# Kernel tuning notes

Hardware: AMD Instinct MI355X
Metric: run time of the kernel (lower is better)

## Reference

```python
import jax, jax.numpy as jnp
import numpy as np

D_MODEL = 512
EXPAND = 2
D_INNER = D_MODEL * EXPAND      # 1024
STATE = 64                      # N
DT_RANK = D_MODEL // 16         # 32
CONV_K = 4
K_WIN = 8                       # window of the approximate selective scan
LN_EPS = 1e-5


def setup_inputs() -> dict:
    key = jax.random.key(0)
    ks = jax.random.split(key, 8)
    norm = lambda k, shape, scale: (jax.random.normal(k, shape, jnp.float32) * scale)
    return {
        "x": jax.random.normal(ks[0], (1, 1024, D_MODEL), jnp.float32),
        "in_proj_w": norm(ks[1], (2 * D_INNER, D_MODEL), D_MODEL ** -0.5),
        "conv_w": norm(ks[2], (D_INNER, 1, CONV_K), 0.5),            # depthwise [O, I/g=1, K]
        "conv_b": jnp.zeros((D_INNER,), jnp.float32),
        "x_proj_w": norm(ks[3], (DT_RANK + 2 * STATE, D_INNER), D_INNER ** -0.5),
        "dt_proj_w": norm(ks[4], (D_INNER, DT_RANK), DT_RANK ** -0.5),
        "dt_proj_b": jnp.zeros((D_INNER,), jnp.float32),
        "A_log": jnp.broadcast_to(
            jnp.log(jnp.arange(1, STATE + 1, dtype=jnp.float32)), (D_INNER, STATE)
        ) + 0.0,
        "D_param": jnp.ones((D_INNER,), jnp.float32),
        "out_proj_w": norm(ks[5], (D_MODEL, D_INNER), D_INNER ** -0.5),
        "ln_w": jnp.ones((D_MODEL,), jnp.float32),
        "ln_b": jnp.zeros((D_MODEL,), jnp.float32),
    }


def _selective_scan(x, dt, A, Bp, Cp, Dp):
    """Windowed selective scan (faithful to the torch loop, vectorized).

    h_t = sum_{s=max(0,t-K+1)}^{t} exp(sum_{j=s+1}^{t} dt_j * A) * dt_s * B_s * x_s
    y_t = <h_t, C_t> + D * x_t
    x, dt: [B, L, d]; A: [d, N]; Bp, Cp: [B, L, N]; Dp: [d]
    """
    L = x.shape[1]
    K = min(L, K_WIN)
    log_dA = dt[..., None] * A                                # [B,L,d,N], <= 0
    dBx = dt[..., None] * Bp[:, :, None, :] * x[..., None]    # [B,L,d,N]
    cs = jnp.cumsum(log_dA, axis=1)                           # prefix sums of log-decay
    h = dBx
    for k in range(1, K):  # fixed small window, 7 iterations
        decay = jnp.exp(cs[:, k:] - cs[:, :-k])               # prod dA over (t-k, t]
        h = h.at[:, k:].add(decay * dBx[:, :-k])
    y = jnp.einsum('bldn,bln->bld', h, Cp) + Dp * x
    return y


def reference(x, in_proj_w, conv_w, conv_b, x_proj_w, dt_proj_w, dt_proj_b,
              A_log, D_param, out_proj_w, ln_w, ln_b):
    residual = x
    xz = x @ in_proj_w.T                                      # [B,L,2*d_inner]
    x_in, z = jnp.split(xz, 2, axis=-1)

    # causal depthwise conv1d (torch pads 3 both sides then keeps first L)
    xc = jnp.transpose(x_in, (0, 2, 1))                       # [B,d,L]
    xc = jax.lax.conv_general_dilated(
        xc, conv_w, window_strides=(1,), padding=[(CONV_K - 1, 0)],
        dimension_numbers=('NCH', 'OIH', 'NCH'), feature_group_count=D_INNER,
    ) + conv_b[None, :, None]
    xc = jax.nn.silu(jnp.transpose(xc, (0, 2, 1)))            # [B,L,d]

    x_dbl = xc @ x_proj_w.T                                   # [B,L,dt_rank+2N]
    dt, Bp, Cp = jnp.split(x_dbl, [DT_RANK, DT_RANK + STATE], axis=-1)
    dt = jax.nn.softplus(dt @ dt_proj_w.T + dt_proj_b)        # [B,L,d]
    A = -jnp.exp(A_log)                                       # [d,N]

    y = _selective_scan(xc, dt, A, Bp, Cp, D_param)
    y = y * jax.nn.silu(z)
    out = y @ out_proj_w.T + residual

    mu = out.mean(-1, keepdims=True)
    var = ((out - mu) ** 2).mean(-1, keepdims=True)
    return (out - mu) * jax.lax.rsqrt(var + LN_EPS) * ln_w + ln_b
```

## Files before the change

### kernel.cpp

```cpp
#include <hip/hip_runtime.h>
#include <hip/hip_fp16.h>
#include <math.h>

#define LSEQ    1024
#define DMODEL  512
#define DINNER  1024
#define NSTATE  64
#define NFUSED  1152
#define CHUNKT  64
#define PROWS   72
#define NCH     16

#define MB (1024u * 1024u)
#define XZ_OFF      (0)
#define XC_OFF      (8u * MB)
#define XCBF_OFF    (12u * MB)
#define XBF_OFF     (14u * MB)
#define INWBF_OFF   (15u * MB)
#define OUTWBF_OFF  (17u * MB)
#define WF_OFF      (18u * MB)
#define FUSED_OFF   (20u * MB + 256u * 1024)
#define BCHI_OFF    (24u * MB + 768u * 1024)
#define YBF_OFF     (25u * MB)
#define OUTPRE_OFF  (27u * MB)

typedef __attribute__((ext_vector_type(8))) short bf16x8;
typedef __attribute__((ext_vector_type(4))) float f32x4;

__device__ inline unsigned short f2bf(float f) {
  unsigned int u = __float_as_uint(f);
  u += 0x7fff + ((u >> 16) & 1);
  return (unsigned short)(u >> 16);
}
__device__ inline float h2f(unsigned short h) {
  return __half2float(__ushort_as_half(h));
}
__device__ inline float fexp2(float x) { return __builtin_amdgcn_exp2f(x); }

__global__ __launch_bounds__(256) void prep_kernel(
    const float* __restrict__ x, const float* __restrict__ inw,
    const float* __restrict__ outw, const float* __restrict__ xpw,
    const float* __restrict__ dtw, unsigned short* __restrict__ x_bf,
    unsigned short* __restrict__ inw_bf, unsigned short* __restrict__ outw_bf,
    unsigned short* __restrict__ Wf) {
  const int blk = blockIdx.x;
  if (blk < 2048) {
    const int i = blk * 256 + threadIdx.x;
    const float* src;
    unsigned short* dst;
    int j;
    if (i < 131072) {
      src = x; dst = x_bf; j = i;
    } else if (i < 393216) {
      src = inw; dst = inw_bf; j = i - 131072;
    } else {
      src = outw; dst = outw_bf; j = i - 393216;
    }
    const float4 v = *(const float4*)&src[(size_t)j * 4];
    ushort4 o;
    o.x = f2bf(v.x); o.y = f2bf(v.y); o.z = f2bf(v.z); o.w = f2bf(v.w);
    *(ushort4*)&dst[(size_t)j * 4] = o;
  } else {
    const int r = blk - 2048;
    if (r < 128) {
      for (int i = threadIdx.x; i < 1024; i += 256)
        Wf[(size_t)r * 1024 + i] = f2bf(xpw[(size_t)(32 + r) * 1024 + i]);
    } else {
      const int d = r - 128;
      __shared__ float w[32];
      if (threadIdx.x < 32) w[threadIdx.x] = dtw[d * 32 + threadIdx.x];
      __syncthreads();
      for (int i = threadIdx.x; i < 1024; i += 256) {
        float s = 0.f;
#pragma unroll
        for (int q = 0; q < 32; ++q) s = fmaf(w[q], xpw[(size_t)q * 1024 + i], s);
        Wf[(size_t)r * 1024 + i] = f2bf(s);
      }
    }
  }
}

template <int BM, int BN, int WM, int WN, bool RESID, bool WBCH>
__global__ __launch_bounds__(256) void gemm_bf(
    const unsigned short* __restrict__ A, const unsigned short* __restrict__ B,
    float* __restrict__ C, const float* __restrict__ resid,
    unsigned short* __restrict__ bch, int M, int N, int K) {
  constexpr int BK = 64;
  constexpr int WTM = BM / WM;
  constexpr int WTN = BN / WN;
  constexpr int FM = WTM / 16;
  constexpr int FN = WTN / 16;
  constexpr int APASS = (BM * BK * 2) / 4096;
  constexpr int BPASS = (BN * BK * 2) / 4096;

  __shared__ unsigned short As[2][BM * BK];
  __shared__ unsigned short Bs[2][BN * BK];

  const int tid = threadIdx.x;
  const int lane = tid & 63;
  const int wave = tid >> 6;
  const int wr = (wave / WN) * WTM;
  const int wc = (wave % WN) * WTN;
  const int bm = blockIdx.y * BM;
  const int bn = blockIdx.x * BN;

  auto stage = [&](int buf, int kt) {
#pragma unroll
    for (int p = 0; p < APASS; ++p) {
      const int s = tid + p * 256;
      const int row = s >> 3;
      const int sch = (s & 7) ^ (row & 7);
      const unsigned short* src = A + (size_t)(bm + row) * K + kt + sch * 8;
      __builtin_amdgcn_global_load_lds(
          (const __attribute__((address_space(1))) unsigned int*)src,
          (__attribute__((address_space(3))) unsigned int*)(&As[buf][s * 8]),
          16, 0, 0);
    }
#pragma unroll
    for (int p = 0; p < BPASS; ++p) {
      const int s = tid + p * 256;
      const int row = s >> 3;
      const int sch = (s & 7) ^ (row & 7);
      const unsigned short* src = B + (size_t)(bn + row) * K + kt + sch * 8;
      __builtin_amdgcn_global_load_lds(
          (const __attribute__((address_space(1))) unsigned int*)src,
          (__attribute__((address_space(3))) unsigned int*)(&Bs[buf][s * 8]),
          16, 0, 0);
    }
  };

  f32x4 acc[FM][FN];
#pragma unroll
  for (int m = 0; m < FM; ++m)
#pragma unroll
    for (int n = 0; n < FN; ++n) acc[m][n] = (f32x4){0.f, 0.f, 0.f, 0.f};

  const int nt = K / BK;
  stage(0, 0);
  __syncthreads();
  int cur = 0;
  for (int t = 0; t < nt; ++t) {
    if (t + 1 < nt) stage(cur ^ 1, (t + 1) * BK);
#pragma unroll
    for (int kk = 0; kk < BK / 32; ++kk) {
      bf16x8 a[FM], b[FN];
#pragma unroll
      for (int m = 0; m < FM; ++m) {
        const int arow = wr + m * 16 + (lane & 15);
        const int ach = (kk * 4 + (lane >> 4)) ^ (arow & 7);
        a[m] = *(const bf16x8*)(&As[cur][arow * BK + ach * 8]);
      }
#pragma unroll
      for (int n = 0; n < FN; ++n) {
        const int brow = wc + n * 16 + (lane & 15);
        const int bchk = (kk * 4 + (lane >> 4)) ^ (brow & 7);
        b[n] = *(const bf16x8*)(&Bs[cur][brow * BK + bchk * 8]);
      }
#pragma unroll
      for (int m = 0; m < FM; ++m)
#pragma unroll
        for (int n = 0; n < FN; ++n)
          acc[m][n] = __builtin_amdgcn_mfma_f32_16x16x32_bf16(a[m], b[n],
                                                              acc[m][n], 0, 0, 0);
    }
    __syncthreads();
    cur ^= 1;
  }

#pragma unroll
  for (int m = 0; m < FM; ++m)
#pragma unroll
    for (int n = 0; n < FN; ++n) {
      const int col = bn + wc + n * 16 + (lane & 15);
#pragma unroll
      for (int r = 0; r < 4; ++r) {
        const int row = bm + wr + m * 16 + (lane >> 4) * 4 + r;
        float v = acc[m][n][r];
        if (RESID) v += resid[(size_t)row * N + col];
        C[(size_t)row * N + col] = v;
        if (WBCH) {
          if (col < 128) {
            const int j = col & 63, hi = col >> 6;
            bch[(size_t)row * 128 + j * 2 + hi] =
                __half_as_ushort(__float2half(v));
          }
        }
      }
    }
}

__global__ __launch_bounds__(256) void conv_silu_kernel(
    const float* __restrict__ xz, const float* __restrict__ w,
    const float* __restrict__ b, float* __restrict__ xc,
    unsigned short* __restrict__ xc_bf) {
  const int idx = blockIdx.x * 256 + threadIdx.x;
  const int t = idx >> 10;
  const int d = idx & 1023;
  float acc = b[d];
#pragma unroll
  for (int j = 0; j < 4; ++j) {
    const int ts = t - 3 + j;
    if (ts >= 0) acc = fmaf(xz[(size_t)ts * 2048 + d], w[d * 4 + j], acc);
  }
  const float s = acc / (1.f + __expf(-acc));
  xc[idx] = s;
  xc_bf[idx] = f2bf(s);
}

__global__ __launch_bounds__(512) void scan_kernel(
    const float* __restrict__ fused,
    const unsigned int* __restrict__ bchi,
    const float* __restrict__ xc,
    const float* __restrict__ xz,
    const float* __restrict__ A_log,
    const float* __restrict__ dtb,
    const float* __restrict__ Dp,
    unsigned short* __restrict__ y_bf) {
  __shared__ unsigned int bch[PROWS * 64];
  __shared__ float2 dtl[PROWS * NCH];
  __shared__ unsigned int auxl[CHUNKT * NCH];
  __shared__ unsigned short ytile[CHUNKT * NCH];

  const int tid = threadIdx.x;
  const int lane = tid & 63;
  const int wave = tid >> 6;
  const int d0 = blockIdx.x * NCH;
  const int t0 = blockIdx.y * CHUNKT;
  const int T = t0 - 8;

#pragma unroll
  for (int pp = 0; pp < 3; ++pp) {
    const int idx = pp * 512 + tid;
    if (idx < PROWS * 16) {
      const int p = idx >> 4;
      const int c4 = (idx & 15) * 4;
      const int gt = T + p;
      uint4 v = make_uint4(0u, 0u, 0u, 0u);
      if (gt >= 0) v = *(const uint4*)&bchi[(size_t)gt * 64 + c4];
      *(uint4*)&bch[p * 64 + c4] = v;
    }
  }

  if (tid < 4 * PROWS) {
    const int row = tid >> 2;
    const int dloc = (tid & 3) * 4;
    const int gt = T + row;
    if (gt >= 0) {
      const float4 f  = *(const float4*)&fused[(size_t)gt * NFUSED + 128 + d0 + dloc];
      const float4 xv = *(const float4*)&xc[(size_t)gt * DINNER + d0 + dloc];
      const float4 zv = *(const float4*)&xz[(size_t)gt * 2048 + DINNER + d0 + dloc];
      const float4 dp = *(const float4*)&Dp[d0 + dloc];
      const float4 db = *(const float4*)&dtb[d0 + dloc];
      const float fa[4] = {f.x, f.y, f.z, f.w};
      const float xa[4] = {xv.x, xv.y, xv.z, xv.w};
      const float za[4] = {zv.x, zv.y, zv.z, zv.w};
      const float pa[4] = {dp.x, dp.y, dp.z, dp.w};
      const float ba[4] = {db.x, db.y, db.z, db.w};
#pragma unroll
      for (int q = 0; q < 4; ++q) {
        const float dtp = fa[q] + ba[q];
        const float dt = (dtp > 20.f) ? dtp : __logf(1.f + __expf(dtp));
        dtl[row * NCH + dloc + q] = make_float2(dt, dt * xa[q]);
        if (row >= 8) {
          const float dxc = pa[q] * xa[q];
          const float sz = za[q] / (1.f + __expf(-za[q]));
          auxl[(row - 8) * NCH + dloc + q] =
              (unsigned int)__half_as_ushort(__float2half(dxc)) |
              ((unsigned int)__half_as_ushort(__float2half(sz)) << 16);
        }
      }
    } else {
#pragma unroll
      for (int q = 0; q < 4; ++q)
        dtl[row * NCH + dloc + q] = make_float2(0.f, 0.f);
    }
  }
  __syncthreads();

  const int chl = wave * 2;
  const float An2a = -__expf(A_log[(size_t)(d0 + chl) * NSTATE + lane]) * 1.44269504f;
  const float An2b = -__expf(A_log[(size_t)(d0 + chl + 1) * NSTATE + lane]) * 1.44269504f;

  float ERa[8], dBa[8], ERb[8], dBb[8];
#pragma unroll
  for (int p = 0; p < 8; ++p) {
    const float4 pk = *(const float4*)&dtl[p * NCH + chl];
    const float Bp = h2f((unsigned short)(bch[p * 64 + lane] & 0xffffu));
    ERa[p] = fexp2(An2a * pk.x);
    dBa[p] = pk.y * Bp;
    ERb[p] = fexp2(An2b * pk.z);
    dBb[p] = pk.w * Bp;
  }

  for (int sb = 0; sb < CHUNKT; sb += 8) {
#pragma unroll
    for (int qu = 0; qu < 2; ++qu) {
      float cc[8];
#pragma unroll
      for (int h4 = 0; h4 < 4; ++h4) {
        const int u = qu * 4 + h4;
        const int p = sb + 8 + u;
        const float4 pk = *(const float4*)&dtl[p * NCH + chl];
        const unsigned int bc = bch[p * 64 + lane];
        const float Bp = h2f((unsigned short)(bc & 0xffffu));
        const float Cp = h2f((unsigned short)(bc >> 16));
        const float Ea = fexp2(An2a * pk.x);
        const float Eb = fexp2(An2b * pk.z);
        const float dBta = pk.y * Bp;
        const float dBtb = pk.w * Bp;

        float sa = dBa[(u - 7) & 7];
        float sb2 = dBb[(u - 7) & 7];
#pragma unroll
        for (int k = 6; k >= 1; --k) {
          const int sl = (u - k) & 7;
          sa = fmaf(ERa[sl], sa, dBa[sl]);
          sb2 = fmaf(ERb[sl], sb2, dBb[sl]);
        }
        const float ha = fmaf(Ea, sa, dBta);
        const float hb = fmaf(Eb, sb2, dBtb);
        ERa[u] = Ea; dBa[u] = dBta;
        ERb[u] = Eb; dBb[u] = dBtb;
        cc[h4 * 2] = ha * Cp;
        cc[h4 * 2 + 1] = hb * Cp;
      }
      float a[8];
#pragma unroll
      for (int i = 0; i < 8; ++i) a[i] = cc[i] + __shfl_xor(cc[i], 1, 64);
      float b0 = (lane & 1) ? a[1] : a[0];
      float b1 = (lane & 1) ? a[3] : a[2];
      float b2 = (lane & 1) ? a[5] : a[4];
      float b3 = (lane & 1) ? a[7] : a[6];
      b0 += __shfl_xor(b0, 2, 64);
      b1 += __shfl_xor(b1, 2, 64);
      b2 += __shfl_xor(b2, 2, 64);
      b3 += __shfl_xor(b3, 2, 64);
      float c0 = (lane & 2) ? b1 : b0;
      float c1 = (lane & 2) ? b3 : b2;
      c0 += __shfl_xor(c0, 4, 64);
      c1 += __shfl_xor(c1, 4, 64);
      float r = (lane & 4) ? c1 : c0;
      r += __shfl_xor(r, 8, 64);
      r += __shfl_xor(r, 16, 64);
      r += __shfl_xor(r, 32, 64);
      if (lane < 8) {
        const int s = sb + qu * 4 + (lane >> 1);
        const int ch = chl + (lane & 1);
        const unsigned int av = auxl[s * NCH + ch];
        const float dxc = h2f((unsigned short)(av & 0xffffu));
        const float sz  = h2f((unsigned short)(av >> 16));
        ytile[s * NCH + ch] = f2bf((r + dxc) * sz);
      }
    }
  }

  __syncthreads();
  {
    const int t = tid >> 3;
    const int c2 = (tid & 7) * 2;
    const unsigned int vy = *(const unsigned int*)&ytile[t * NCH + c2];
    *(unsigned int*)&y_bf[(size_t)(t0 + t) * DINNER + d0 + c2] = vy;
  }
}

__global__ __launch_bounds__(256) void ln_kernel(
    const float* __restrict__ src, const float* __restrict__ w,
    const float* __restrict__ b, float* __restrict__ out) {
  const int t = blockIdx.x;
  const int i0 = threadIdx.x;
  const int i1 = threadIdx.x + 256;
  const float v0 = src[(size_t)t * DMODEL + i0];
  const float v1 = src[(size_t)t * DMODEL + i1];
  float s = v0 + v1;
  float q = v0 * v0 + v1 * v1;
#pragma unroll
  for (int m = 32; m; m >>= 1) {
    s += __shfl_xor(s, m, 64);
    q += __shfl_xor(q, m, 64);
  }
  __shared__ float ss[4], sq[4];
  const int wv = threadIdx.x >> 6;
  if ((threadIdx.x & 63) == 0) { ss[wv] = s; sq[wv] = q; }
  __syncthreads();
  s = ss[0] + ss[1] + ss[2] + ss[3];
  q = sq[0] + sq[1] + sq[2] + sq[3];
  const float mu = s * (1.f / 512.f);
  const float var = q * (1.f / 512.f) - mu * mu;
  const float inv = rsqrtf(var + 1e-5f);
  out[(size_t)t * DMODEL + i0] = (v0 - mu) * inv * w[i0] + b[i0];
  out[(size_t)t * DMODEL + i1] = (v1 - mu) * inv * w[i1] + b[i1];
}

extern "C" void kernel_launch(void* const* d_in, const int* in_sizes, int n_in,
                              void* d_out, int out_size, void* d_ws,
                              size_t ws_size, hipStream_t stream) {
  const float* x         = (const float*)d_in[0];
  const float* in_w      = (const float*)d_in[1];
  const float* conv_w    = (const float*)d_in[2];
  const float* conv_b    = (const float*)d_in[3];
  const float* xproj_w   = (const float*)d_in[4];
  const float* dtproj_w  = (const float*)d_in[5];
  const float* dtproj_b  = (const float*)d_in[6];
  const float* A_log     = (const float*)d_in[7];
  const float* Dp        = (const float*)d_in[8];
  const float* outproj_w = (const float*)d_in[9];
  const float* ln_w      = (const float*)d_in[10];
  const float* ln_b      = (const float*)d_in[11];
  float* out = (float*)d_out;

  char* ws = (char*)d_ws;
  float*          xz      = (float*)(ws + XZ_OFF);
  float*          xc      = (float*)(ws + XC_OFF);
  unsigned short* xc_bf   = (unsigned short*)(ws + XCBF_OFF);
  unsigned short* x_bf    = (unsigned short*)(ws + XBF_OFF);
  unsigned short* inw_bf  = (unsigned short*)(ws + INWBF_OFF);
  unsigned short* outw_bf = (unsigned short*)(ws + OUTWBF_OFF);
  unsigned short* Wf      = (unsigned short*)(ws + WF_OFF);
  float*          fused   = (float*)(ws + FUSED_OFF);
  unsigned short* bchi    = (unsigned short*)(ws + BCHI_OFF);
  unsigned short* y_bf    = (unsigned short*)(ws + YBF_OFF);
  float*          outpre  = (float*)(ws + OUTPRE_OFF);

  prep_kernel<<<3200, 256, 0, stream>>>(x, in_w, outproj_w, xproj_w, dtproj_w,
                                        x_bf, inw_bf, outw_bf, Wf);
  gemm_bf<64, 64, 2, 2, false, false>
      <<<dim3(2048 / 64, 1024 / 64), 256, 0, stream>>>(
          x_bf, inw_bf, xz, nullptr, nullptr, 1024, 2048, 512);
  conv_silu_kernel<<<(LSEQ * DINNER) / 256, 256, 0, stream>>>(xz, conv_w,
                                                              conv_b, xc, xc_bf);
  gemm_bf<64, 64, 2, 2, false, true>
      <<<dim3(NFUSED / 64, 1024 / 64), 256, 0, stream>>>(
          xc_bf, Wf, fused, nullptr, bchi, 1024, NFUSED, 1024);
  scan_kernel<<<dim3(DINNER / NCH, LSEQ / CHUNKT), 512, 0, stream>>>(
      fused, (const unsigned int*)bchi, xc, xz, A_log, dtproj_b, Dp, y_bf);
  gemm_bf<32, 32, 2, 2, true, false>
      <<<dim3(512 / 32, 1024 / 32), 256, 0, stream>>>(
          y_bf, outw_bf, outpre, x, nullptr, 1024, 512, 1024);
  ln_kernel<<<LSEQ, 256, 0, stream>>>(outpre, ln_w, ln_b, out);
}
```

Measured before the change: 94.16 us.

## Vectorize conv kernel, batch dt weight folding, halve scan chunk length

The conv+SiLU kernel now handles four channels per thread with float4 loads and stores, and the prep kernel folds eight dt_proj rows per block so each x_proj column is loaded once and reused. The scan chunk length drops from 64 to 32 timesteps, which doubles the number of scan blocks for better occupancy. The price is more halo overhead: each 32-step chunk loads 8 extra rows, against 8 per 64 before.

```diff
diff --git a/kernel.cpp b/kernel.cpp
--- a/kernel.cpp
+++ b/kernel.cpp
@@ -7,8 +7,8 @@
 #define DINNER  1024
 #define NSTATE  64
 #define NFUSED  1152
-#define CHUNKT  64
-#define PROWS   72
+#define CHUNKT  32
+#define PROWS   40
 #define NCH     16
 
 #define MB (1024u * 1024u)
@@ -60,21 +60,26 @@
     ushort4 o;
     o.x = f2bf(v.x); o.y = f2bf(v.y); o.z = f2bf(v.z); o.w = f2bf(v.w);
     *(ushort4*)&dst[(size_t)j * 4] = o;
+  } else if (blk < 2176) {
+    const int r = blk - 2048;
+    for (int i = threadIdx.x; i < 1024; i += 256)
+      Wf[(size_t)r * 1024 + i] = f2bf(xpw[(size_t)(32 + r) * 1024 + i]);
   } else {
-    const int r = blk - 2048;
-    if (r < 128) {
-      for (int i = threadIdx.x; i < 1024; i += 256)
-        Wf[(size_t)r * 1024 + i] = f2bf(xpw[(size_t)(32 + r) * 1024 + i]);
-    } else {
-      const int d = r - 128;
-      __shared__ float w[32];
-      if (threadIdx.x < 32) w[threadIdx.x] = dtw[d * 32 + threadIdx.x];
-      __syncthreads();
-      for (int i = threadIdx.x; i < 1024; i += 256) {
+    const int dbase = (blk - 2176) * 8;
+    __shared__ float w8[8][32];
+    w8[threadIdx.x >> 5][threadIdx.x & 31] =
+        dtw[(size_t)(dbase + (threadIdx.x >> 5)) * 32 + (threadIdx.x & 31)];
+    __syncthreads();
+    for (int i = threadIdx.x; i < 1024; i += 256) {
+      float xv[32];
+#pragma unroll
+      for (int q = 0; q < 32; ++q) xv[q] = xpw[(size_t)q * 1024 + i];
+#pragma unroll
+      for (int dd = 0; dd < 8; ++dd) {
         float s = 0.f;
 #pragma unroll
-        for (int q = 0; q < 32; ++q) s = fmaf(w[q], xpw[(size_t)q * 1024 + i], s);
-        Wf[(size_t)r * 1024 + i] = f2bf(s);
+        for (int q = 0; q < 32; ++q) s = fmaf(w8[dd][q], xv[q], s);
+        Wf[(size_t)(128 + dbase + dd) * 1024 + i] = f2bf(s);
       }
     }
   }
@@ -193,18 +198,38 @@
     const float* __restrict__ xz, const float* __restrict__ w,
     const float* __restrict__ b, float* __restrict__ xc,
     unsigned short* __restrict__ xc_bf) {
-  const int idx = blockIdx.x * 256 + threadIdx.x;
-  const int t = idx >> 10;
-  const int d = idx & 1023;
-  float acc = b[d];
+  const int idx4 = blockIdx.x * 256 + threadIdx.x;
+  const int t = idx4 >> 8;
+  const int d4 = (idx4 & 255) << 2;
+
+  float4 wv[4];
+#pragma unroll
+  for (int dd = 0; dd < 4; ++dd) wv[dd] = *(const float4*)&w[(d4 + dd) * 4];
+  const float4 bv = *(const float4*)&b[d4];
+  float acc[4] = {bv.x, bv.y, bv.z, bv.w};
+
 #pragma unroll
   for (int j = 0; j < 4; ++j) {
     const int ts = t - 3 + j;
-    if (ts >= 0) acc = fmaf(xz[(size_t)ts * 2048 + d], w[d * 4 + j], acc);
-  }
-  const float s = acc / (1.f + __expf(-acc));
-  xc[idx] = s;
-  xc_bf[idx] = f2bf(s);
+    if (ts >= 0) {
+      const float4 xv = *(const float4*)&xz[(size_t)ts * 2048 + d4];
+      const float xs[4] = {xv.x, xv.y, xv.z, xv.w};
+#pragma unroll
+      for (int dd = 0; dd < 4; ++dd)
+        acc[dd] = fmaf(xs[dd], ((const float*)&wv[dd])[j], acc[dd]);
+    }
+  }
+  float4 o;
+  ushort4 ob;
+  float* op = (float*)&o;
+#pragma unroll
+  for (int dd = 0; dd < 4; ++dd) {
+    const float s = acc[dd] / (1.f + __expf(-acc[dd]));
+    op[dd] = s;
+    ((unsigned short*)&ob)[dd] = f2bf(s);
+  }
+  *(float4*)&xc[(size_t)t * DINNER + d4] = o;
+  *(ushort4*)&xc_bf[(size_t)t * DINNER + d4] = ob;
 }
 
 __global__ __launch_bounds__(512) void scan_kernel(
@@ -229,7 +254,7 @@
   const int T = t0 - 8;
 
 #pragma unroll
-  for (int pp = 0; pp < 3; ++pp) {
+  for (int pp = 0; pp < 2; ++pp) {
     const int idx = pp * 512 + tid;
     if (idx < PROWS * 16) {
       const int p = idx >> 4;
@@ -355,7 +380,7 @@
   }
 
   __syncthreads();
-  {
+  if (tid < CHUNKT * 8) {
     const int t = tid >> 3;
     const int c2 = (tid & 7) * 2;
     const unsigned int vy = *(const unsigned int*)&ytile[t * NCH + c2];
@@ -421,13 +446,12 @@
   unsigned short* y_bf    = (unsigned short*)(ws + YBF_OFF);
   float*          outpre  = (float*)(ws + OUTPRE_OFF);
 
-  prep_kernel<<<3200, 256, 0, stream>>>(x, in_w, outproj_w, xproj_w, dtproj_w,
+  prep_kernel<<<2304, 256, 0, stream>>>(x, in_w, outproj_w, xproj_w, dtproj_w,
                                         x_bf, inw_bf, outw_bf, Wf);
   gemm_bf<64, 64, 2, 2, false, false>
       <<<dim3(2048 / 64, 1024 / 64), 256, 0, stream>>>(
           x_bf, inw_bf, xz, nullptr, nullptr, 1024, 2048, 512);
-  conv_silu_kernel<<<(LSEQ * DINNER) / 256, 256, 0, stream>>>(xz, conv_w,
-                                                              conv_b, xc, xc_bf);
+  conv_silu_kernel<<<1024, 256, 0, stream>>>(xz, conv_w, conv_b, xc, xc_bf);
   gemm_bf<64, 64, 2, 2, false, true>
       <<<dim3(NFUSED / 64, 1024 / 64), 256, 0, stream>>>(
           xc_bf, Wf, fused, nullptr, bchi, 1024, NFUSED, 1024);
```

Result: no change. 94.24 us (+0.1%).
